# Performance work log

Measured on AMD Instinct MI355X. Metric: run time of the kernel, lower is better.

## Reference

```python
import jax, jax.numpy as jnp
import numpy as np

B, N, H = 1024, 200, 64


def setup_inputs() -> dict:
    key = jax.random.key(0)
    ks = jax.random.split(key, 8)
    A = jax.random.uniform(ks[0], (B, 2 * N, N), dtype=jnp.float32)
    hidden = jax.random.normal(ks[1], (B, N, H), dtype=jnp.float32)
    s = 1.0 / np.sqrt(H)
    w_ih = jax.random.normal(ks[2], (3 * H, 2 * H), dtype=jnp.float32) * s
    w_hh = jax.random.normal(ks[3], (3 * H, H), dtype=jnp.float32) * s
    b_ih = jnp.zeros((3 * H,), jnp.float32)
    b_hh = jnp.zeros((3 * H,), jnp.float32)
    b_iah = jnp.zeros((H,), jnp.float32)
    b_oah = jnp.zeros((H,), jnp.float32)
    W_in = jax.random.normal(ks[4], (H, H), dtype=jnp.float32) * s
    bias_in = jnp.zeros((H,), jnp.float32)
    W_out = jax.random.normal(ks[5], (H, H), dtype=jnp.float32) * s
    bias_out = jnp.zeros((H,), jnp.float32)
    return {"A": A, "hidden": hidden, "w_ih": w_ih, "w_hh": w_hh,
            "b_ih": b_ih, "b_hh": b_hh, "b_iah": b_iah, "b_oah": b_oah,
            "W_in": W_in, "bias_in": bias_in, "W_out": W_out, "bias_out": bias_out}


def reference(A, hidden, w_ih, w_hh, b_ih, b_hh, b_iah, b_oah,
              W_in, bias_in, W_out, bias_out):
    # SessionGNN._cell, step=1.
    n = A.shape[1] // 2
    A_in, A_out = A[:, :n, :], A[:, n:, :]          # (B, N, N) each
    h_in = jnp.einsum('bnh,gh->bng', hidden, W_in) + bias_in    # (B, N, H)
    h_out = jnp.einsum('bnh,gh->bng', hidden, W_out) + bias_out
    input_in = jnp.matmul(A_in, h_in) + b_iah       # (B, N, H)
    input_out = jnp.matmul(A_out, h_out) + b_oah
    inputs = jnp.concatenate([input_in, input_out], axis=2)     # (B, N, 2H)
    gi = jnp.einsum('bni,gi->bng', inputs, w_ih) + b_ih         # (B, N, 3H)
    gh = jnp.einsum('bnh,gh->bng', hidden, w_hh) + b_hh
    i_r, i_i, i_n = jnp.split(gi, 3, axis=2)
    h_r, h_i, h_n = jnp.split(gh, 3, axis=2)
    resetgate = jax.nn.sigmoid(i_r + h_r)
    inputgate = jax.nn.sigmoid(i_i + h_i)
    newgate = jnp.tanh(i_n + resetgate * h_n)
    return hidden - inputgate * (hidden - newgate)
```

## Files before the change

### kernel.cpp

```cpp
#include <hip/hip_runtime.h>

typedef _Float16 f16;
typedef __attribute__((ext_vector_type(4))) _Float16 f16x4;
typedef __attribute__((ext_vector_type(8))) _Float16 f16x8;
typedef __attribute__((ext_vector_type(4))) float f32x4;

#define MFMA16(a, b, c) __builtin_amdgcn_mfma_f32_16x16x32_f16((a), (b), (c), 0, 0, 0)

__device__ __forceinline__ f16x8 cvt8(float4 a, float4 b) {
    f16x8 r;
    r[0] = (f16)a.x; r[1] = (f16)a.y; r[2] = (f16)a.z; r[3] = (f16)a.w;
    r[4] = (f16)b.x; r[5] = (f16)b.y; r[6] = (f16)b.z; r[7] = (f16)b.w;
    return r;
}

__device__ __forceinline__ f16x8 zero8() {
    f16x8 z;
#pragma unroll
    for (int q = 0; q < 8; ++q) z[q] = (f16)0.0f;
    return z;
}

__global__ void prep_kernel(const float* __restrict__ w_ih, const float* __restrict__ w_hh,
                            const float* __restrict__ b_ih, const float* __restrict__ b_hh,
                            const float* __restrict__ b_iah, const float* __restrict__ b_oah,
                            const float* __restrict__ W_in, const float* __restrict__ bias_in,
                            const float* __restrict__ W_out, const float* __restrict__ bias_out,
                            f16* __restrict__ Wc, f16* __restrict__ Whh, f16* __restrict__ Wih,
                            float* __restrict__ cstA, float* __restrict__ cstB,
                            float* __restrict__ biasc) {
    const int gid = blockIdx.x * 256 + threadIdx.x;
    const int gstride = gridDim.x * 256;
    for (int i = gid; i < 8192; i += gstride)
        Wc[i] = (f16)(i < 4096 ? W_in[i] : W_out[i - 4096]);
    for (int i = gid; i < 12288; i += gstride) Whh[i] = (f16)w_hh[i];
    for (int i = gid; i < 24576; i += gstride) Wih[i] = (f16)w_ih[i];
    for (int job = gid; job < 768; job += gstride) {
        const int g = job >> 2, q = job & 3;
        float s = (q == 0) ? b_ih[g] : 0.0f;
        const float* wr = w_ih + g * 128 + q * 32;
        for (int i = 0; i < 32; ++i)
            s += wr[i] * ((q * 32 + i < 64) ? b_iah[q * 32 + i] : b_oah[q * 32 + i - 64]);
        atomicAdd(&cstA[g], s);
    }
    for (int g = gid; g < 192; g += gstride) cstB[g] = b_hh[g];
    for (int j = gid; j < 128; j += gstride) biasc[j] = (j < 64) ? bias_in[j] : bias_out[j - 64];
}

__global__ void zero_kernel(float* __restrict__ cstA) {
    if (threadIdx.x < 192) cstA[threadIdx.x] = 0.0f;
}

__global__ __launch_bounds__(512, 2) void gru_fused(
    const float* __restrict__ A, const float* __restrict__ hidden,
    const f16* __restrict__ Wc, const f16* __restrict__ Whh, const f16* __restrict__ Wih,
    const float* __restrict__ cstA, const float* __restrict__ cstB,
    const float* __restrict__ biasc, float* __restrict__ out) {
    __shared__ __align__(16) char lds_raw[63232];
    f16* hT  = (f16*)lds_raw;
    f16* inp = (f16*)lds_raw;

    const int b = blockIdx.x;
    const float* Ab = A + (size_t)b * 80000;
    const float* hb = hidden + (size_t)b * 12800;
    float* ob = out + (size_t)b * 12800;

    const int tid = threadIdx.x;
    const int w   = tid >> 6;
    const int l   = tid & 63;
    const int l15 = l & 15;
    const int lg  = l >> 4;

    for (int mt = w; mt < 13; mt += 8) {
        const int m  = mt * 16 + l15;
        const int mc = m < 200 ? m : 199;
        const float* hrow = hb + mc * 64;
        float4 r0 = *(const float4*)(hrow + lg * 8);
        float4 r1 = *(const float4*)(hrow + lg * 8 + 4);
        float4 r2 = *(const float4*)(hrow + 32 + lg * 8);
        float4 r3 = *(const float4*)(hrow + 32 + lg * 8 + 4);
        f16x8 a0 = cvt8(r0, r1), a1 = cvt8(r2, r3);
        const int m0 = mt * 16 + lg * 4;
#pragma unroll
        for (int jt = 0; jt < 8; ++jt) {
            const int j = jt * 16 + l15;
            f32x4 acc = {0.f, 0.f, 0.f, 0.f};
            acc = MFMA16(a0, *(const f16x8*)(Wc + j * 64 + lg * 8), acc);
            acc = MFMA16(a1, *(const f16x8*)(Wc + j * 64 + 32 + lg * 8), acc);
            const float bc = biasc[j];
            if (m0 < 200) {
                f16x4 pk;
                pk[0] = (f16)(acc[0] + bc); pk[1] = (f16)(acc[1] + bc);
                pk[2] = (f16)(acc[2] + bc); pk[3] = (f16)(acc[3] + bc);
                *(f16x4*)(hT + j * 200 + m0) = pk;
            }
        }
    }
    __syncthreads();

    const int g  = w & 3;
    const int rg = w >> 2;
    const int hf = g >> 1;
    f16x8 B0[7], B1[7];
    {
        const f16* hT0 = hT + (g * 32 + l15) * 200;
        const f16* hT1 = hT + (g * 32 + 16 + l15) * 200;
#pragma unroll
        for (int ks = 0; ks < 6; ++ks) {
            B0[ks] = *(const f16x8*)(hT0 + ks * 32 + lg * 8);
            B1[ks] = *(const f16x8*)(hT1 + ks * 32 + lg * 8);
        }
        B0[6] = (lg == 0) ? *(const f16x8*)(hT0 + 192) : zero8();
        B1[6] = (lg == 0) ? *(const f16x8*)(hT1 + 192) : zero8();
    }
    __syncthreads();

#define AROWP(T) (Ab + (size_t)(hf * 200 + ((((T) * 16 + l15) < 200) ? ((T) * 16 + l15) : 199)) * 200)

    float4 p[2][2];

#define PHASE2(TBEG, NT)                                                          \
    {                                                                             \
        const float* ap0 = AROWP(TBEG) + lg * 8;                                  \
        p[0][0] = *(const float4*)ap0;                                            \
        p[0][1] = *(const float4*)(ap0 + 4);                                      \
        const float* ap1 = AROWP(TBEG) + 32 + lg * 8;                             \
        p[1][0] = *(const float4*)ap1;                                            \
        p[1][1] = *(const float4*)(ap1 + 4);                                      \
        _Pragma("unroll")                                                         \
        for (int tt = 0; tt < (NT); ++tt) {                                       \
            const int t = (TBEG) + tt;                                            \
            f32x4 a0 = {0.f, 0.f, 0.f, 0.f}, a1 = {0.f, 0.f, 0.f, 0.f};           \
            _Pragma("unroll")                                                     \
            for (int k = 0; k < 7; ++k) {                                         \
                const int s = tt * 7 + k;                                         \
                float4 q0 = p[s & 1][0], q1 = p[s & 1][1];                        \
                const int ns = s + 2, nt = ns / 7, nk = ns % 7;                   \
                if (nt < (NT)) {                                                  \
                    const float* ap = AROWP((TBEG) + nt)                          \
                                      + (nk < 6 ? nk * 32 + lg * 8 : 192);        \
                    p[s & 1][0] = *(const float4*)ap;                             \
                    p[s & 1][1] = *(const float4*)(ap + 4);                       \
                }                                                                 \
                f16x8 af = (k == 6 && lg != 0) ? zero8() : cvt8(q0, q1);          \
                a0 = MFMA16(af, B0[k], a0);                                       \
                a1 = MFMA16(af, B1[k], a1);                                       \
            }                                                                     \
            _Pragma("unroll")                                                     \
            for (int r = 0; r < 4; ++r) {                                         \
                const int n = t * 16 + lg * 4 + r;                                \
                if (n < 200) {                                                    \
                    inp[n * 152 + g * 32 + l15]      = (f16)a0[r];                \
                    inp[n * 152 + g * 32 + 16 + l15] = (f16)a1[r];                \
                }                                                                 \
            }                                                                     \
        }                                                                         \
    }

    if (rg == 0) PHASE2(0, 7) else PHASE2(7, 6)
#undef PHASE2
#undef AROWP
    __syncthreads();

    const int c    = w & 3;
    const int wm2  = w >> 2;
    const int hcol = c * 16 + l15;
    f16x8 Wf0[4], Wf1[4], Wf2[4];
#pragma unroll
    for (int k = 0; k < 4; ++k) {
        Wf0[k] = *(const f16x8*)(Wih + (hcol      ) * 128 + k * 32 + lg * 8);
        Wf1[k] = *(const f16x8*)(Wih + (64  + hcol) * 128 + k * 32 + lg * 8);
        Wf2[k] = *(const f16x8*)(Wih + (128 + hcol) * 128 + k * 32 + lg * 8);
    }
    f16x8 Hf0[2], Hf1[2], Hf2[2];
#pragma unroll
    for (int k = 0; k < 2; ++k) {
        Hf0[k] = *(const f16x8*)(Whh + (hcol      ) * 64 + k * 32 + lg * 8);
        Hf1[k] = *(const f16x8*)(Whh + (64  + hcol) * 64 + k * 32 + lg * 8);
        Hf2[k] = *(const f16x8*)(Whh + (128 + hcol) * 64 + k * 32 + lg * 8);
    }
    const float cAr = cstA[hcol], cAi = cstA[64 + hcol], cAn = cstA[128 + hcol];
    const float cBr = cstB[hcol], cBi = cstB[64 + hcol], cBn = cstB[128 + hcol];

    for (int t = wm2; t < 13; t += 2) {
        const int n  = t * 16 + l15;
        const int nc = n < 200 ? n : 199;
        f32x4 gir = {0.f,0.f,0.f,0.f}, gii = {0.f,0.f,0.f,0.f}, gin = {0.f,0.f,0.f,0.f};
        f32x4 ghr = {0.f,0.f,0.f,0.f}, ghi = {0.f,0.f,0.f,0.f}, ghn = {0.f,0.f,0.f,0.f};
#pragma unroll
        for (int k = 0; k < 2; ++k) {
            const int h = k * 32 + lg * 8;
            float4 r0 = *(const float4*)(hb + nc * 64 + h);
            float4 r1 = *(const float4*)(hb + nc * 64 + h + 4);
            f16x8 a = cvt8(r0, r1);
            ghr = MFMA16(a, Hf0[k], ghr);
            ghi = MFMA16(a, Hf1[k], ghi);
            ghn = MFMA16(a, Hf2[k], ghn);
        }
#pragma unroll
        for (int k = 0; k < 4; ++k) {
            f16x8 a = *(const f16x8*)(inp + nc * 152 + k * 32 + lg * 8);
            gir = MFMA16(a, Wf0[k], gir);
            gii = MFMA16(a, Wf1[k], gii);
            gin = MFMA16(a, Wf2[k], gin);
        }
#pragma unroll
        for (int r = 0; r < 4; ++r) {
            const int row = t * 16 + lg * 4 + r;
            if (row < 200) {
                const float hv = hb[row * 64 + hcol];
                const float xr = gir[r] + ghr[r] + cAr + cBr;
                const float xi = gii[r] + ghi[r] + cAi + cBi;
                const float rg2 = 1.0f / (1.0f + __expf(-xr));
                const float ig = 1.0f / (1.0f + __expf(-xi));
                const float xn = gin[r] + cAn + rg2 * (ghn[r] + cBn);
                const float e2 = __expf(2.0f * xn);
                const float ng = 1.0f - 2.0f / (e2 + 1.0f);
                ob[row * 64 + hcol] = hv + ig * (ng - hv);
            }
        }
    }
}

extern "C" void kernel_launch(void* const* d_in, const int* in_sizes, int n_in,
                              void* d_out, int out_size, void* d_ws, size_t ws_size,
                              hipStream_t stream) {
    const float* A        = (const float*)d_in[0];
    const float* hidden   = (const float*)d_in[1];
    const float* w_ih     = (const float*)d_in[2];
    const float* w_hh     = (const float*)d_in[3];
    const float* b_ih     = (const float*)d_in[4];
    const float* b_hh     = (const float*)d_in[5];
    const float* b_iah    = (const float*)d_in[6];
    const float* b_oah    = (const float*)d_in[7];
    const float* W_in     = (const float*)d_in[8];
    const float* bias_in  = (const float*)d_in[9];
    const float* W_out    = (const float*)d_in[10];
    const float* bias_out = (const float*)d_in[11];
    float* out = (float*)d_out;

    char* wsb = (char*)d_ws;
    f16* Wc      = (f16*)wsb;
    f16* Whh     = Wc + 8192;
    f16* Wih     = Whh + 12288;
    float* cstA  = (float*)(wsb + 90112);
    float* cstB  = cstA + 192;
    float* biasc = cstB + 192;

    zero_kernel<<<dim3(1), dim3(256), 0, stream>>>(cstA);
    prep_kernel<<<dim3(64), dim3(256), 0, stream>>>(
        w_ih, w_hh, b_ih, b_hh, b_iah, b_oah, W_in, bias_in, W_out, bias_out,
        Wc, Whh, Wih, cstA, cstB, biasc);
    gru_fused<<<dim3(1024), dim3(512), 0, stream>>>(
        A, hidden, Wc, Whh, Wih, cstA, cstB, biasc, out);
}
```

Before: 169.3 us.

## Repartition A×h matmul so each wave owns all 64 columns of one half

Phase 2 is restructured so each wave handles one adjacency half (in or out) and an interleaved set of row tiles across all 64 output columns, instead of 32 columns over half the row tiles. A rows are read once per wave per tile rather than twice across waves, halving global A traffic. B fragments are now read from LDS inside the loop instead of being held in registers. Results are buffered in registers and written to LDS after a barrier, so the input buffer can alias hT and the LDS footprint shrinks. The cost is more LDS reads and more live registers for the buffered outputs.

```diff
diff --git a/kernel.cpp b/kernel.cpp
--- a/kernel.cpp
+++ b/kernel.cpp
@@ -51,12 +51,55 @@
     if (threadIdx.x < 192) cstA[threadIdx.x] = 0.0f;
 }
 
+template<int NT>
+__device__ __forceinline__ void phase2_run(const float* const rp[4], const f16* hTb,
+                                           const int lg, f16x4 pk[4][4]) {
+    float4 p[2][2];
+    p[0][0] = *(const float4*)(rp[0] + lg * 8);
+    p[0][1] = *(const float4*)(rp[0] + lg * 8 + 4);
+    p[1][0] = *(const float4*)(rp[0] + 32 + lg * 8);
+    p[1][1] = *(const float4*)(rp[0] + 32 + lg * 8 + 4);
+    f32x4 acc[4];
+#pragma unroll
+    for (int s = 0; s < NT * 7; ++s) {
+        const int tt = s / 7, k = s % 7;
+        float4 q0 = p[s & 1][0], q1 = p[s & 1][1];
+        const int ns = s + 2;
+        if (ns < NT * 7) {
+            const int nt_ = ns / 7, nk = ns % 7;
+            const float* ap = rp[nt_] + (nk < 6 ? nk * 32 + lg * 8 : 192);
+            p[s & 1][0] = *(const float4*)ap;
+            p[s & 1][1] = *(const float4*)(ap + 4);
+        }
+        if (k == 0) {
+#pragma unroll
+            for (int c = 0; c < 4; ++c) acc[c] = (f32x4){0.f, 0.f, 0.f, 0.f};
+        }
+        f16x8 af = (k == 6 && lg != 0) ? zero8() : cvt8(q0, q1);
+        const int koffB = (k == 6) ? 192 : k * 32 + lg * 8;
+#pragma unroll
+        for (int c = 0; c < 4; ++c) {
+            const f16x8 bf = *(const f16x8*)(hTb + c * 3200 + koffB);
+            acc[c] = MFMA16(af, bf, acc[c]);
+        }
+        if (k == 6) {
+#pragma unroll
+            for (int c = 0; c < 4; ++c) {
+                f16x4 t;
+                t[0] = (f16)acc[c][0]; t[1] = (f16)acc[c][1];
+                t[2] = (f16)acc[c][2]; t[3] = (f16)acc[c][3];
+                pk[tt][c] = t;
+            }
+        }
+    }
+}
+
 __global__ __launch_bounds__(512, 2) void gru_fused(
     const float* __restrict__ A, const float* __restrict__ hidden,
     const f16* __restrict__ Wc, const f16* __restrict__ Whh, const f16* __restrict__ Wih,
     const float* __restrict__ cstA, const float* __restrict__ cstB,
     const float* __restrict__ biasc, float* __restrict__ out) {
-    __shared__ __align__(16) char lds_raw[63232];
+    __shared__ __align__(16) char lds_raw[60800];
     f16* hT  = (f16*)lds_raw;
     f16* inp = (f16*)lds_raw;
 
@@ -89,77 +132,46 @@
             acc = MFMA16(a1, *(const f16x8*)(Wc + j * 64 + 32 + lg * 8), acc);
             const float bc = biasc[j];
             if (m0 < 200) {
-                f16x4 pk;
-                pk[0] = (f16)(acc[0] + bc); pk[1] = (f16)(acc[1] + bc);
-                pk[2] = (f16)(acc[2] + bc); pk[3] = (f16)(acc[3] + bc);
-                *(f16x4*)(hT + j * 200 + m0) = pk;
+                f16x4 pkk;
+                pkk[0] = (f16)(acc[0] + bc); pkk[1] = (f16)(acc[1] + bc);
+                pkk[2] = (f16)(acc[2] + bc); pkk[3] = (f16)(acc[3] + bc);
+                *(f16x4*)(hT + j * 200 + m0) = pkk;
             }
         }
     }
     __syncthreads();
 
-    const int g  = w & 3;
-    const int rg = w >> 2;
-    const int hf = g >> 1;
-    f16x8 B0[7], B1[7];
-    {
-        const f16* hT0 = hT + (g * 32 + l15) * 200;
-        const f16* hT1 = hT + (g * 32 + 16 + l15) * 200;
-#pragma unroll
-        for (int ks = 0; ks < 6; ++ks) {
-            B0[ks] = *(const f16x8*)(hT0 + ks * 32 + lg * 8);
-            B1[ks] = *(const f16x8*)(hT1 + ks * 32 + lg * 8);
-        }
-        B0[6] = (lg == 0) ? *(const f16x8*)(hT0 + 192) : zero8();
-        B1[6] = (lg == 0) ? *(const f16x8*)(hT1 + 192) : zero8();
-    }
+    const int hf = w >> 2;
+    const int q  = w & 3;
+    const float* rp[4];
+#pragma unroll
+    for (int ti = 0; ti < 4; ++ti) {
+        const int t = q + 4 * ti;
+        int row = t * 16 + l15;
+        if (row > 199) row = 199;
+        rp[ti] = Ab + (size_t)(hf * 200 + row) * 200;
+    }
+    const f16* hTb = hT + (hf * 64 + l15) * 200;
+
+    f16x4 pk[4][4];
+    if (q == 0) phase2_run<4>(rp, hTb, lg, pk);
+    else        phase2_run<3>(rp, hTb, lg, pk);
     __syncthreads();
 
-#define AROWP(T) (Ab + (size_t)(hf * 200 + ((((T) * 16 + l15) < 200) ? ((T) * 16 + l15) : 199)) * 200)
-
-    float4 p[2][2];
-
-#define PHASE2(TBEG, NT)                                                          \
-    {                                                                             \
-        const float* ap0 = AROWP(TBEG) + lg * 8;                                  \
-        p[0][0] = *(const float4*)ap0;                                            \
-        p[0][1] = *(const float4*)(ap0 + 4);                                      \
-        const float* ap1 = AROWP(TBEG) + 32 + lg * 8;                             \
-        p[1][0] = *(const float4*)ap1;                                            \
-        p[1][1] = *(const float4*)(ap1 + 4);                                      \
-        _Pragma("unroll")                                                         \
-        for (int tt = 0; tt < (NT); ++tt) {                                       \
-            const int t = (TBEG) + tt;                                            \
-            f32x4 a0 = {0.f, 0.f, 0.f, 0.f}, a1 = {0.f, 0.f, 0.f, 0.f};           \
-            _Pragma("unroll")                                                     \
-            for (int k = 0; k < 7; ++k) {                                         \
-                const int s = tt * 7 + k;                                         \
-                float4 q0 = p[s & 1][0], q1 = p[s & 1][1];                        \
-                const int ns = s + 2, nt = ns / 7, nk = ns % 7;                   \
-                if (nt < (NT)) {                                                  \
-                    const float* ap = AROWP((TBEG) + nt)                          \
-                                      + (nk < 6 ? nk * 32 + lg * 8 : 192);        \
-                    p[s & 1][0] = *(const float4*)ap;                             \
-                    p[s & 1][1] = *(const float4*)(ap + 4);                       \
-                }                                                                 \
-                f16x8 af = (k == 6 && lg != 0) ? zero8() : cvt8(q0, q1);          \
-                a0 = MFMA16(af, B0[k], a0);                                       \
-                a1 = MFMA16(af, B1[k], a1);                                       \
-            }                                                                     \
-            _Pragma("unroll")                                                     \
-            for (int r = 0; r < 4; ++r) {                                         \
-                const int n = t * 16 + lg * 4 + r;                                \
-                if (n < 200) {                                                    \
-                    inp[n * 152 + g * 32 + l15]      = (f16)a0[r];                \
-                    inp[n * 152 + g * 32 + 16 + l15] = (f16)a1[r];                \
-                }                                                                 \
-            }                                                                     \
-        }                                                                         \
-    }
-
-    if (rg == 0) PHASE2(0, 7) else PHASE2(7, 6)
-#undef PHASE2
-#undef AROWP
+    const int NT = (q == 0) ? 4 : 3;
+#pragma unroll
+    for (int ti = 0; ti < 4; ++ti) {
+        if (ti < NT) {
+#pragma unroll
+            for (int c = 0; c < 4; ++c) {
+#pragma unroll
+                for (int r = 0; r < 4; ++r) {
+                    const int n = (q + 4 * ti) * 16 + lg * 4 + r;
+                    if (n < 200) inp[n * 152 + hf * 64 + c * 16 + l15] = pk[ti][c][r];
+                }
+            }
+        }
+    }
     __syncthreads();
 
     const int c    = w & 3;
```

New measurement: 194.0 us. 14.6% more time.
